# Kernel tuning notes

Measured on AMD Instinct MI355X. Metric: run time of the kernel, lower is better.

The kernel has to match this reference:

```python
import jax, jax.numpy as jnp
import numpy as np

EMBED = 1024
HEADS = 16
HEAD_DIM = EMBED // HEADS
SCALE = HEAD_DIM ** -0.5


def setup_inputs() -> dict:
    key = jax.random.key(0)
    ks = jax.random.split(key, 9)
    init = lambda k, shape: jax.random.normal(k, shape, dtype=jnp.float32) * 0.02
    return {
        "hidden_states": jax.random.normal(ks[0], (32, 257, EMBED), dtype=jnp.float32),
        "Wq": init(ks[1], (EMBED, EMBED)), "bq": init(ks[2], (EMBED,)),
        "Wk": init(ks[3], (EMBED, EMBED)), "bk": init(ks[4], (EMBED,)),
        "Wv": init(ks[5], (EMBED, EMBED)), "bv": init(ks[6], (EMBED,)),
        "Wo": init(ks[7], (EMBED, EMBED)), "bo": init(ks[8], (EMBED,)),
    }


def reference(hidden_states, Wq, bq, Wk, bk, Wv, bv, Wo, bo):
    b, t, d = hidden_states.shape
    # projections (torch Linear: x @ W.T + b); scale applied to Q
    q = (hidden_states @ Wq.T + bq) * SCALE
    k = hidden_states @ Wk.T + bk
    v = hidden_states @ Wv.T + bv
    # [b, h, t, hd]
    q = q.reshape(b, t, HEADS, HEAD_DIM).transpose(0, 2, 1, 3)
    k = k.reshape(b, t, HEADS, HEAD_DIM).transpose(0, 2, 1, 3)
    v = v.reshape(b, t, HEADS, HEAD_DIM).transpose(0, 2, 1, 3)
    # attention scores + softmax (dropout p is a no-op in eval mode)
    scores = jnp.einsum("bhqd,bhkd->bhqk", q, k)
    probs = jax.nn.softmax(scores, axis=-1)
    ctx = jnp.einsum("bhqk,bhkd->bhqd", probs, v)
    ctx = ctx.transpose(0, 2, 1, 3).reshape(b, t, d)
    return ctx @ Wo.T + bo
```

## Files before the change

kernel.cpp:

```cpp
#include <hip/hip_runtime.h>


#define B_   32
#define T_   257
#define TP   272
#define H_   16
#define HD_  64
#define D_   1024
#define NTOK 8224
#define BH_  512
#define FRAG_PER_BH 17408

typedef __bf16 bf16;
typedef __bf16 bf16x4 __attribute__((ext_vector_type(4)));
typedef __bf16 bf16x8 __attribute__((ext_vector_type(8)));
typedef short  s16x4  __attribute__((ext_vector_type(4)));
typedef short  s16x8  __attribute__((ext_vector_type(8)));
typedef float  floatx4 __attribute__((ext_vector_type(4)));

static constexpr size_t SZ_XB   = (size_t)NTOK * D_ * 2;
static constexpr size_t SZ_WQKV = (size_t)3 * D_ * D_ * 2;
static constexpr size_t SZ_W    = (size_t)D_ * D_ * 2;
static constexpr size_t SZ_QK   = (size_t)BH_ * FRAG_PER_BH * 2;

static constexpr size_t OFF_XB   = 0;
static constexpr size_t OFF_WQKV = OFF_XB + SZ_XB;
static constexpr size_t OFF_WO   = OFF_WQKV + SZ_WQKV;
static constexpr size_t OFF_Q    = OFF_WO + SZ_W;
static constexpr size_t OFF_K    = OFF_Q + SZ_QK;
static constexpr size_t OFF_V    = OFF_K + SZ_QK;
static constexpr size_t OFF_CTX  = OFF_V + SZ_QK;

#define GLD16(gp, lp)                                                        \
  __builtin_amdgcn_global_load_lds(                                          \
      (const __attribute__((address_space(1))) void*)(gp),                   \
      (__attribute__((address_space(3))) void*)(lp), 16, 0, 0)

__global__ void cast_bf16_kernel(const float* __restrict__ src,
                                 bf16* __restrict__ dst, int n4) {
  int i = blockIdx.x * blockDim.x + threadIdx.x;
  int stride = gridDim.x * blockDim.x;
  for (int idx = i; idx < n4; idx += stride) {
    float4 v = reinterpret_cast<const float4*>(src)[idx];
    bf16x4 o;
    o[0] = (bf16)v.x; o[1] = (bf16)v.y; o[2] = (bf16)v.z; o[3] = (bf16)v.w;
    reinterpret_cast<bf16x4*>(dst)[idx] = o;
  }
}

__global__ void cast4_kernel(const float* __restrict__ s0, const float* __restrict__ s1,
                             const float* __restrict__ s2, const float* __restrict__ s3,
                             bf16* __restrict__ d0, bf16* __restrict__ d1,
                             bf16* __restrict__ d2, bf16* __restrict__ d3, int n4) {
  const float* s = (blockIdx.y == 0) ? s0 : (blockIdx.y == 1) ? s1
                   : (blockIdx.y == 2) ? s2 : s3;
  bf16* d = (blockIdx.y == 0) ? d0 : (blockIdx.y == 1) ? d1
            : (blockIdx.y == 2) ? d2 : d3;
  int i = blockIdx.x * blockDim.x + threadIdx.x;
  int stride = gridDim.x * blockDim.x;
  for (int idx = i; idx < n4; idx += stride) {
    float4 v = reinterpret_cast<const float4*>(s)[idx];
    bf16x4 o;
    o[0] = (bf16)v.x; o[1] = (bf16)v.y; o[2] = (bf16)v.z; o[3] = (bf16)v.w;
    reinterpret_cast<bf16x4*>(d)[idx] = o;
  }
}


__global__ __launch_bounds__(256) void qkv_gemm(
    const bf16* __restrict__ xb, const bf16* __restrict__ wqkv,
    const float* __restrict__ bq, const float* __restrict__ bk,
    const float* __restrict__ bv,
    bf16* __restrict__ Qf, bf16* __restrict__ Kf, bf16* __restrict__ Vf) {
  __shared__ bf16 smem[9216];
  bf16* Ash = smem;
  bf16* Bsh = smem + 4096;

  const int linear = blockIdx.x;
  const int nbg = ((linear & 7) * 3 + ((linear >> 3) % 3)) * 128;
  const int mbase = (linear / 24) * 128;
  const int tid = threadIdx.x;
  const int lane = tid & 63;
  const int w = tid >> 6;
  const int wr = w >> 1, wc = w & 1;
  const int n15 = lane & 15, quad = lane >> 4;

  const int lrow = lane >> 2;
  const int lseg = (lane & 3) * 8;

  floatx4 acc[4][4] = {};

  for (int k0 = 0; k0 < D_; k0 += 32) {
#pragma unroll
    for (int c = 0; c < 2; c++) {
      int r0 = w * 32 + c * 16;
      int row = r0 + lrow;
      int gm = mbase + row; if (gm > NTOK - 1) gm = NTOK - 1;
      GLD16(xb + (size_t)gm * D_ + k0 + lseg, Ash + r0 * 32);
      GLD16(wqkv + (size_t)(nbg + row) * D_ + k0 + lseg, Bsh + r0 * 32);
    }
    __syncthreads();
    bf16x8 af[4], bfr[4];
#pragma unroll
    for (int i = 0; i < 4; i++) {
      af[i]  = *reinterpret_cast<const bf16x8*>(Ash + (wr * 64 + i * 16 + n15) * 32 + quad * 8);
      bfr[i] = *reinterpret_cast<const bf16x8*>(Bsh + (wc * 64 + i * 16 + n15) * 32 + quad * 8);
    }
#pragma unroll
    for (int i = 0; i < 4; i++)
#pragma unroll
      for (int j = 0; j < 4; j++)
        acc[i][j] = __builtin_amdgcn_mfma_f32_16x16x32_bf16(af[i], bfr[j], acc[i][j], 0, 0, 0);
    __syncthreads();
  }

  const int z = nbg >> 10;
  bf16* zdst = (z == 0) ? Qf : (z == 1) ? Kf : Vf;
  const float scale = (z == 0) ? 0.125f : 1.0f;
  const float* bias = (z == 0) ? bq : (z == 1) ? bk : bv;
  const int zoff = nbg & 1023;

  const int bA = mbase / T_;
  const int tA = mbase - bA * T_;
  const int tEndA = (tA + 128 < T_) ? tA + 128 : T_;
  const int tgA0 = tA >> 4;
  const int nA = ((tEndA - 1) >> 4) - tgA0 + 1;
  int nU = nA, tEndB = 0;
  if (tA + 128 > T_ && bA + 1 < B_) {
    tEndB = tA + 128 - T_;
    nU += ((tEndB - 1) >> 4) + 1;
  }

  for (int half = 0; half < 2; half++) {
    if (wc == half) {
#pragma unroll
      for (int i = 0; i < 4; i++)
#pragma unroll
        for (int j = 0; j < 4; j++) {
          int colL = j * 16 + n15;
          float bval = bias[zoff + half * 64 + colL];
#pragma unroll
          for (int r = 0; r < 4; r++) {
            int rowL = wr * 64 + i * 16 + quad * 4 + r;
            smem[rowL * 72 + colL] = (bf16)((acc[i][j][r] + bval) * scale);
          }
        }
    }
    __syncthreads();
    const int h = (zoff >> 6) + half;
    for (int u = w; u < nU; u += 4) {
      int b, tg, tlo, thi;
      if (u < nA) {
        b = bA; tg = tgA0 + u;
        tlo = (tA > tg * 16) ? tA : tg * 16;
        int te = tg * 16 + 16; thi = (te < tEndA) ? te : tEndA;
      } else {
        b = bA + 1; tg = u - nA;
        tlo = tg * 16;
        int te = tg * 16 + 16; thi = (te < tEndB) ? te : tEndB;
      }
      bf16* gb = zdst + (size_t)(b * H_ + h) * FRAG_PER_BH + tg * 1024;
      if (z != 2) {
        int ki = lane & 15, dc = lane >> 4;
        int t = tg * 16 + ki;
        if (t >= tlo && t < thi) {
          int rowL = b * T_ + t - mbase;
          bf16x8 v0 = *reinterpret_cast<const bf16x8*>(smem + rowL * 72 + dc * 8);
          bf16x8 v1 = *reinterpret_cast<const bf16x8*>(smem + rowL * 72 + 32 + dc * 8);
          *reinterpret_cast<bf16x8*>(gb + dc * 128 + ki * 8) = v0;
          *reinterpret_cast<bf16x8*>(gb + 512 + dc * 128 + ki * 8) = v1;
        }
      } else {
        int q2 = (lane >> 4) & 3, d16 = lane & 15;
        int tb = tg * 16 + q2 * 4;
        bool full = (tb >= tlo) && (tb + 3 < thi);
#pragma unroll
        for (int p = 0; p < 2; p++) {
          bf16x8 vv;
#pragma unroll
          for (int dp = 0; dp < 2; dp++)
#pragma unroll
            for (int ki = 0; ki < 4; ki++) {
              int t = tb + ki;
              int rr = (b * T_ + t - mbase) & 127;
              vv[dp * 4 + ki] = smem[rr * 72 + p * 32 + dp * 16 + d16];
            }
          bf16* cp = gb + (p * 4 + q2) * 128 + d16 * 8;
          if (full) {
            *reinterpret_cast<bf16x8*>(cp) = vv;
          } else {
#pragma unroll
            for (int dp = 0; dp < 2; dp++)
#pragma unroll
              for (int ki = 0; ki < 4; ki++) {
                int t = tb + ki;
                if (t >= tlo && t < thi) cp[dp * 4 + ki] = vv[dp * 4 + ki];
              }
          }
        }
      }
    }
    __syncthreads();
  }
}

__global__ __launch_bounds__(256) void attn_kernel(
    const bf16* __restrict__ Qf, const bf16* __restrict__ Kf,
    const bf16* __restrict__ Vf, bf16* __restrict__ ctx) {
  __shared__ bf16 smem[34816];

  const int bh = blockIdx.x;
  const int tid = threadIdx.x;
  const int lane = tid & 63, w = tid >> 6;
  const int n15 = lane & 15, quad = lane >> 4;
  const int b = bh >> 4, h = bh & 15;

  const bf16* Qb = Qf + (size_t)bh * FRAG_PER_BH;
  const bf16* Kb = Kf + (size_t)bh * FRAG_PER_BH;
  const bf16* Vb = Vf + (size_t)bh * FRAG_PER_BH;

#pragma unroll
  for (int j = 0; j < 17; j++) {
    int c = w * 17 + j;
    const bf16* src = (c < 34) ? (Kb + c * 512) : (Vb + (c - 34) * 512);
    GLD16(src + lane * 8, smem + c * 512);
  }
  __syncthreads();
  const bf16* Ksh = smem;
  const bf16* Vsh = smem + 17408;

  const int fo = quad * 128 + n15 * 8;

  for (int qt = w; qt < 17; qt += 4) {
    bf16x8 qb0 = *reinterpret_cast<const bf16x8*>(Qb + qt * 1024 + fo);
    bf16x8 qb1 = *reinterpret_cast<const bf16x8*>(Qb + qt * 1024 + 512 + fo);

    floatx4 s[17];
#pragma unroll
    for (int kt = 0; kt < 17; kt++) {
      bf16x8 ka0 = *reinterpret_cast<const bf16x8*>(Ksh + kt * 1024 + fo);
      bf16x8 ka1 = *reinterpret_cast<const bf16x8*>(Ksh + kt * 1024 + 512 + fo);
      floatx4 c = {};
      c = __builtin_amdgcn_mfma_f32_16x16x32_bf16(ka0, qb0, c, 0, 0, 0);
      c = __builtin_amdgcn_mfma_f32_16x16x32_bf16(ka1, qb1, c, 0, 0, 0);
      s[kt] = c;
    }
    s[16][1] = -1e30f; s[16][2] = -1e30f; s[16][3] = -1e30f;
    if (quad != 0) s[16][0] = -1e30f;

    float m0 = -1e30f;
#pragma unroll
    for (int kt = 0; kt < 17; kt++)
#pragma unroll
      for (int r = 0; r < 4; r++) m0 = fmaxf(m0, s[kt][r]);
    m0 = fmaxf(m0, __shfl_xor(m0, 16));
    m0 = fmaxf(m0, __shfl_xor(m0, 32));

    float sum = 0.f;
    s16x4 pb[17];
#pragma unroll
    for (int kt = 0; kt < 17; kt++) {
      bf16x4 ph;
#pragma unroll
      for (int r = 0; r < 4; r++) {
        float p = __expf(s[kt][r] - m0);
        sum += p;
        ph[r] = (bf16)p;
      }
      pb[kt] = __builtin_bit_cast(s16x4, ph);
    }
    sum += __shfl_xor(sum, 16);
    sum += __shfl_xor(sum, 32);

    floatx4 o[4] = {};
#pragma unroll
    for (int kt = 0; kt < 17; kt++) {
#pragma unroll
      for (int p = 0; p < 2; p++) {
        bf16x8 vv = *reinterpret_cast<const bf16x8*>(
            Vsh + ((kt * 2 + p) * 4 + quad) * 128 + n15 * 8);
        s16x8 v16 = __builtin_bit_cast(s16x8, vv);
        s16x4 vlo = __builtin_shufflevector(v16, v16, 0, 1, 2, 3);
        s16x4 vhi = __builtin_shufflevector(v16, v16, 4, 5, 6, 7);
        o[p * 2]     = __builtin_amdgcn_mfma_f32_16x16x16bf16_1k(vlo, pb[kt], o[p * 2], 0, 0, 0);
        o[p * 2 + 1] = __builtin_amdgcn_mfma_f32_16x16x16bf16_1k(vhi, pb[kt], o[p * 2 + 1], 0, 0, 0);
      }
    }

    int q = qt * 16 + n15;
    if (q < T_) {
      float inv = 1.0f / sum;
      size_t ob = ((size_t)(b * T_ + q)) * D_ + h * 64 + quad * 4;
#pragma unroll
      for (int dt = 0; dt < 4; dt++) {
        bf16x4 ov;
#pragma unroll
        for (int r = 0; r < 4; r++) ov[r] = (bf16)(o[dt][r] * inv);
        *reinterpret_cast<bf16x4*>(ctx + ob + dt * 16) = ov;
      }
    }
  }
}

__global__ __launch_bounds__(256) void o_gemm(
    const bf16* __restrict__ ctx, const bf16* __restrict__ wo,
    const float* __restrict__ bo, float* __restrict__ out) {
  __shared__ bf16 Ash[128 * 32];
  __shared__ bf16 Bsh[128 * 32];

  const int linear = blockIdx.x;
  const int nbase = (linear & 7) * 128;
  const int mbase = (linear >> 3) * 128;
  const int tid = threadIdx.x;
  const int lane = tid & 63;
  const int w = tid >> 6;
  const int wr = w >> 1, wc = w & 1;
  const int n15 = lane & 15, quad = lane >> 4;

  const int lrow = lane >> 2;
  const int lseg = (lane & 3) * 8;

  floatx4 acc[4][4] = {};

  for (int k0 = 0; k0 < D_; k0 += 32) {
#pragma unroll
    for (int c = 0; c < 2; c++) {
      int r0 = w * 32 + c * 16;
      int row = r0 + lrow;
      int gm = mbase + row; if (gm > NTOK - 1) gm = NTOK - 1;
      GLD16(ctx + (size_t)gm * D_ + k0 + lseg, Ash + r0 * 32);
      GLD16(wo + (size_t)(nbase + row) * D_ + k0 + lseg, Bsh + r0 * 32);
    }
    __syncthreads();
    bf16x8 af[4], bfr[4];
#pragma unroll
    for (int i = 0; i < 4; i++) {
      af[i]  = *reinterpret_cast<const bf16x8*>(Ash + (wr * 64 + i * 16 + n15) * 32 + quad * 8);
      bfr[i] = *reinterpret_cast<const bf16x8*>(Bsh + (wc * 64 + i * 16 + n15) * 32 + quad * 8);
    }
#pragma unroll
    for (int i = 0; i < 4; i++)
#pragma unroll
      for (int j = 0; j < 4; j++)
        acc[i][j] = __builtin_amdgcn_mfma_f32_16x16x32_bf16(af[i], bfr[j], acc[i][j], 0, 0, 0);
    __syncthreads();
  }

#pragma unroll
  for (int i = 0; i < 4; i++) {
    int rowb = mbase + wr * 64 + i * 16 + quad * 4;
#pragma unroll
    for (int j = 0; j < 4; j++) {
      int col = nbase + wc * 64 + j * 16 + n15;
      float bval = bo[col];
#pragma unroll
      for (int r = 0; r < 4; r++) {
        int m = rowb + r;
        if (m < NTOK) out[(size_t)m * D_ + col] = acc[i][j][r] + bval;
      }
    }
  }
}

extern "C" void kernel_launch(void* const* d_in, const int* in_sizes, int n_in,
                              void* d_out, int out_size, void* d_ws, size_t ws_size,
                              hipStream_t stream) {
  const float* hs = (const float*)d_in[0];
  const float* Wq = (const float*)d_in[1];
  const float* bq = (const float*)d_in[2];
  const float* Wk = (const float*)d_in[3];
  const float* bk = (const float*)d_in[4];
  const float* Wv = (const float*)d_in[5];
  const float* bv = (const float*)d_in[6];
  const float* Wo = (const float*)d_in[7];
  const float* bo = (const float*)d_in[8];

  char* ws = (char*)d_ws;
  bf16* xb   = (bf16*)(ws + OFF_XB);
  bf16* wqkv = (bf16*)(ws + OFF_WQKV);
  bf16* wob  = (bf16*)(ws + OFF_WO);
  bf16* Qfw  = (bf16*)(ws + OFF_Q);
  bf16* Kfw  = (bf16*)(ws + OFF_K);
  bf16* Vfw  = (bf16*)(ws + OFF_V);
  bf16* ctx  = (bf16*)(ws + OFF_CTX);

  cast_bf16_kernel<<<2048, 256, 0, stream>>>(hs, xb, NTOK * D_ / 4);
  cast4_kernel<<<dim3(256, 4), 256, 0, stream>>>(
      Wq, Wk, Wv, Wo,
      wqkv, wqkv + (size_t)D_ * D_, wqkv + (size_t)2 * D_ * D_, wob,
      D_ * D_ / 4);

  qkv_gemm<<<1560, 256, 0, stream>>>(xb, wqkv, bq, bk, bv, Qfw, Kfw, Vfw);
  attn_kernel<<<BH_, 256, 0, stream>>>(Qfw, Kfw, Vfw, ctx);
  o_gemm<<<520, 256, 0, stream>>>(ctx, wob, bo, (float*)d_out);
}
```

Baseline: 252.1 us.

## Widen GEMM K-tiles with XOR-swizzled LDS, split attention query tiles, use exp2

Both GEMMs now load 64-wide K tiles per iteration into an XOR-swizzled LDS layout, which halves the barrier count and is meant to avoid bank conflicts on fragment reads. The attention kernel splits each (batch, head) across two blocks over query tiles, keeps only K in LDS, and reads V directly from global memory. It also prefetches the next Q fragment. The softmax scale now folds in log2(e) so exp2f replaces __expf. The attention changes double occupancy opportunity but load K twice and rely on cache for the uncached V reads.

```diff
diff --git a/kernel.cpp b/kernel.cpp
--- a/kernel.cpp
+++ b/kernel.cpp
@@ -30,6 +30,8 @@
 static constexpr size_t OFF_K    = OFF_Q + SZ_QK;
 static constexpr size_t OFF_V    = OFF_K + SZ_QK;
 static constexpr size_t OFF_CTX  = OFF_V + SZ_QK;
+
+#define QSCALE 0.18033688011112042f
 
 #define GLD16(gp, lp)                                                        \
   __builtin_amdgcn_global_load_lds(                                          \
@@ -72,9 +74,9 @@
     const float* __restrict__ bq, const float* __restrict__ bk,
     const float* __restrict__ bv,
     bf16* __restrict__ Qf, bf16* __restrict__ Kf, bf16* __restrict__ Vf) {
-  __shared__ bf16 smem[9216];
+  __shared__ bf16 smem[16384];
   bf16* Ash = smem;
-  bf16* Bsh = smem + 4096;
+  bf16* Bsh = smem + 8192;
 
   const int linear = blockIdx.x;
   const int nbg = ((linear & 7) * 3 + ((linear >> 3) % 3)) * 128;
@@ -85,38 +87,47 @@
   const int wr = w >> 1, wc = w & 1;
   const int n15 = lane & 15, quad = lane >> 4;
 
-  const int lrow = lane >> 2;
-  const int lseg = (lane & 3) * 8;
+  const int r8 = lane >> 3;
+  const int sG = ((lane & 7) ^ r8) * 8;
 
   floatx4 acc[4][4] = {};
 
-  for (int k0 = 0; k0 < D_; k0 += 32) {
-#pragma unroll
-    for (int c = 0; c < 2; c++) {
-      int r0 = w * 32 + c * 16;
-      int row = r0 + lrow;
-      int gm = mbase + row; if (gm > NTOK - 1) gm = NTOK - 1;
-      GLD16(xb + (size_t)gm * D_ + k0 + lseg, Ash + r0 * 32);
-      GLD16(wqkv + (size_t)(nbg + row) * D_ + k0 + lseg, Bsh + r0 * 32);
-    }
-    __syncthreads();
-    bf16x8 af[4], bfr[4];
+  for (int k0 = 0; k0 < D_; k0 += 64) {
+#pragma unroll
+    for (int c = 0; c < 4; c++) {
+      int rbase = c * 32 + w * 8;
+      int rloc = rbase + r8;
+      int gm = mbase + rloc; if (gm > NTOK - 1) gm = NTOK - 1;
+      GLD16(xb + (size_t)gm * D_ + k0 + sG, Ash + rbase * 64);
+      GLD16(wqkv + (size_t)(nbg + rloc) * D_ + k0 + sG, Bsh + rbase * 64);
+    }
+    __syncthreads();
+    bf16x8 af[4][2], bfr[4][2];
+    const int sw = n15 & 7;
 #pragma unroll
     for (int i = 0; i < 4; i++) {
-      af[i]  = *reinterpret_cast<const bf16x8*>(Ash + (wr * 64 + i * 16 + n15) * 32 + quad * 8);
-      bfr[i] = *reinterpret_cast<const bf16x8*>(Bsh + (wc * 64 + i * 16 + n15) * 32 + quad * 8);
+      int arow = (wr * 64 + i * 16 + n15) * 64;
+      int brow = (wc * 64 + i * 16 + n15) * 64;
+#pragma unroll
+      for (int hh = 0; hh < 2; hh++) {
+        int so = ((hh * 4 + quad) ^ sw) * 8;
+        af[i][hh]  = *reinterpret_cast<const bf16x8*>(Ash + arow + so);
+        bfr[i][hh] = *reinterpret_cast<const bf16x8*>(Bsh + brow + so);
+      }
     }
 #pragma unroll
     for (int i = 0; i < 4; i++)
 #pragma unroll
-      for (int j = 0; j < 4; j++)
-        acc[i][j] = __builtin_amdgcn_mfma_f32_16x16x32_bf16(af[i], bfr[j], acc[i][j], 0, 0, 0);
+      for (int j = 0; j < 4; j++) {
+        acc[i][j] = __builtin_amdgcn_mfma_f32_16x16x32_bf16(af[i][0], bfr[j][0], acc[i][j], 0, 0, 0);
+        acc[i][j] = __builtin_amdgcn_mfma_f32_16x16x32_bf16(af[i][1], bfr[j][1], acc[i][j], 0, 0, 0);
+      }
     __syncthreads();
   }
 
   const int z = nbg >> 10;
   bf16* zdst = (z == 0) ? Qf : (z == 1) ? Kf : Vf;
-  const float scale = (z == 0) ? 0.125f : 1.0f;
+  const float scale = (z == 0) ? QSCALE : 1.0f;
   const float* bias = (z == 0) ? bq : (z == 1) ? bk : bv;
   const int zoff = nbg & 1023;
 
@@ -207,9 +218,10 @@
 __global__ __launch_bounds__(256) void attn_kernel(
     const bf16* __restrict__ Qf, const bf16* __restrict__ Kf,
     const bf16* __restrict__ Vf, bf16* __restrict__ ctx) {
-  __shared__ bf16 smem[34816];
-
-  const int bh = blockIdx.x;
+  __shared__ bf16 Ksh[17408];
+
+  const int bid = blockIdx.x;
+  const int bh = bid >> 1, z = bid & 1;
   const int tid = threadIdx.x;
   const int lane = tid & 63, w = tid >> 6;
   const int n15 = lane & 15, quad = lane >> 4;
@@ -219,21 +231,26 @@
   const bf16* Kb = Kf + (size_t)bh * FRAG_PER_BH;
   const bf16* Vb = Vf + (size_t)bh * FRAG_PER_BH;
 
-#pragma unroll
-  for (int j = 0; j < 17; j++) {
-    int c = w * 17 + j;
-    const bf16* src = (c < 34) ? (Kb + c * 512) : (Vb + (c - 34) * 512);
-    GLD16(src + lane * 8, smem + c * 512);
-  }
+  for (int j = w; j < 34; j += 4) GLD16(Kb + j * 512 + lane * 8, Ksh + j * 512);
   __syncthreads();
-  const bf16* Ksh = smem;
-  const bf16* Vsh = smem + 17408;
 
   const int fo = quad * 128 + n15 * 8;
-
-  for (int qt = w; qt < 17; qt += 4) {
-    bf16x8 qb0 = *reinterpret_cast<const bf16x8*>(Qb + qt * 1024 + fo);
-    bf16x8 qb1 = *reinterpret_cast<const bf16x8*>(Qb + qt * 1024 + 512 + fo);
+  const int lo = z ? 9 : 0, hi = z ? 17 : 9;
+
+  const int qt0 = lo + w;
+  bf16x8 cq0 = {}, cq1 = {};
+  if (qt0 < hi) {
+    cq0 = *reinterpret_cast<const bf16x8*>(Qb + qt0 * 1024 + fo);
+    cq1 = *reinterpret_cast<const bf16x8*>(Qb + qt0 * 1024 + 512 + fo);
+  }
+
+  for (int qt = qt0; qt < hi; qt += 4) {
+    const int nqt = qt + 4;
+    bf16x8 nq0 = {}, nq1 = {};
+    if (nqt < hi) {
+      nq0 = *reinterpret_cast<const bf16x8*>(Qb + nqt * 1024 + fo);
+      nq1 = *reinterpret_cast<const bf16x8*>(Qb + nqt * 1024 + 512 + fo);
+    }
 
     floatx4 s[17];
 #pragma unroll
@@ -241,8 +258,8 @@
       bf16x8 ka0 = *reinterpret_cast<const bf16x8*>(Ksh + kt * 1024 + fo);
       bf16x8 ka1 = *reinterpret_cast<const bf16x8*>(Ksh + kt * 1024 + 512 + fo);
       floatx4 c = {};
-      c = __builtin_amdgcn_mfma_f32_16x16x32_bf16(ka0, qb0, c, 0, 0, 0);
-      c = __builtin_amdgcn_mfma_f32_16x16x32_bf16(ka1, qb1, c, 0, 0, 0);
+      c = __builtin_amdgcn_mfma_f32_16x16x32_bf16(ka0, cq0, c, 0, 0, 0);
+      c = __builtin_amdgcn_mfma_f32_16x16x32_bf16(ka1, cq1, c, 0, 0, 0);
       s[kt] = c;
     }
     s[16][1] = -1e30f; s[16][2] = -1e30f; s[16][3] = -1e30f;
@@ -263,7 +280,7 @@
       bf16x4 ph;
 #pragma unroll
       for (int r = 0; r < 4; r++) {
-        float p = __expf(s[kt][r] - m0);
+        float p = exp2f(s[kt][r] - m0);
         sum += p;
         ph[r] = (bf16)p;
       }
@@ -278,7 +295,7 @@
 #pragma unroll
       for (int p = 0; p < 2; p++) {
         bf16x8 vv = *reinterpret_cast<const bf16x8*>(
-            Vsh + ((kt * 2 + p) * 4 + quad) * 128 + n15 * 8);
+            Vb + ((kt * 2 + p) * 4 + quad) * 128 + n15 * 8);
         s16x8 v16 = __builtin_bit_cast(s16x8, vv);
         s16x4 vlo = __builtin_shufflevector(v16, v16, 0, 1, 2, 3);
         s16x4 vhi = __builtin_shufflevector(v16, v16, 4, 5, 6, 7);
@@ -299,14 +316,16 @@
         *reinterpret_cast<bf16x4*>(ctx + ob + dt * 16) = ov;
       }
     }
+    cq0 = nq0; cq1 = nq1;
   }
 }
 
 __global__ __launch_bounds__(256) void o_gemm(
     const bf16* __restrict__ ctx, const bf16* __restrict__ wo,
     const float* __restrict__ bo, float* __restrict__ out) {
-  __shared__ bf16 Ash[128 * 32];
-  __shared__ bf16 Bsh[128 * 32];
+  __shared__ bf16 smem[16384];
+  bf16* Ash = smem;
+  bf16* Bsh = smem + 8192;
 
   const int linear = blockIdx.x;
   const int nbase = (linear & 7) * 128;
@@ -317,32 +336,41 @@
   const int wr = w >> 1, wc = w & 1;
   const int n15 = lane & 15, quad = lane >> 4;
 
-  const int lrow = lane >> 2;
-  const int lseg = (lane & 3) * 8;
+  const int r8 = lane >> 3;
+  const int sG = ((lane & 7) ^ r8) * 8;
 
   floatx4 acc[4][4] = {};
 
-  for (int k0 = 0; k0 < D_; k0 += 32) {
-#pragma unroll
-    for (int c = 0; c < 2; c++) {
-      int r0 = w * 32 + c * 16;
-      int row = r0 + lrow;
-      int gm = mbase + row; if (gm > NTOK - 1) gm = NTOK - 1;
-      GLD16(ctx + (size_t)gm * D_ + k0 + lseg, Ash + r0 * 32);
-      GLD16(wo + (size_t)(nbase + row) * D_ + k0 + lseg, Bsh + r0 * 32);
-    }
-    __syncthreads();
-    bf16x8 af[4], bfr[4];
+  for (int k0 = 0; k0 < D_; k0 += 64) {
+#pragma unroll
+    for (int c = 0; c < 4; c++) {
+      int rbase = c * 32 + w * 8;
+      int rloc = rbase + r8;
+      int gm = mbase + rloc; if (gm > NTOK - 1) gm = NTOK - 1;
+      GLD16(ctx + (size_t)gm * D_ + k0 + sG, Ash + rbase * 64);
+      GLD16(wo + (size_t)(nbase + rloc) * D_ + k0 + sG, Bsh + rbase * 64);
+    }
+    __syncthreads();
+    bf16x8 af[4][2], bfr[4][2];
+    const int sw = n15 & 7;
 #pragma unroll
     for (int i = 0; i < 4; i++) {
-      af[i]  = *reinterpret_cast<const bf16x8*>(Ash + (wr * 64 + i * 16 + n15) * 32 + quad * 8);
-      bfr[i] = *reinterpret_cast<const bf16x8*>(Bsh + (wc * 64 + i * 16 + n15) * 32 + quad * 8);
+      int arow = (wr * 64 + i * 16 + n15) * 64;
+      int brow = (wc * 64 + i * 16 + n15) * 64;
+#pragma unroll
+      for (int hh = 0; hh < 2; hh++) {
+        int so = ((hh * 4 + quad) ^ sw) * 8;
+        af[i][hh]  = *reinterpret_cast<const bf16x8*>(Ash + arow + so);
+        bfr[i][hh] = *reinterpret_cast<const bf16x8*>(Bsh + brow + so);
+      }
     }
 #pragma unroll
     for (int i = 0; i < 4; i++)
 #pragma unroll
-      for (int j = 0; j < 4; j++)
-        acc[i][j] = __builtin_amdgcn_mfma_f32_16x16x32_bf16(af[i], bfr[j], acc[i][j], 0, 0, 0);
+      for (int j = 0; j < 4; j++) {
+        acc[i][j] = __builtin_amdgcn_mfma_f32_16x16x32_bf16(af[i][0], bfr[j][0], acc[i][j], 0, 0, 0);
+        acc[i][j] = __builtin_amdgcn_mfma_f32_16x16x32_bf16(af[i][1], bfr[j][1], acc[i][j], 0, 0, 0);
+      }
     __syncthreads();
   }
 
@@ -391,6 +419,6 @@
       D_ * D_ / 4);
 
   qkv_gemm<<<1560, 256, 0, stream>>>(xb, wqkv, bq, bk, bv, Qfw, Kfw, Vfw);
-  attn_kernel<<<BH_, 256, 0, stream>>>(Qfw, Kfw, Vfw, ctx);
+  attn_kernel<<<1024, 256, 0, stream>>>(Qfw, Kfw, Vfw, ctx);
   o_gemm<<<520, 256, 0, stream>>>(ctx, wob, bo, (float*)d_out);
 }
```

Result: slower. 282.9 us (+12.2%).

## Widen attention to 8 waves, fold log2e into Q scale, halve o_gemm M tile

Applied to the files above, without the earlier changes.

Attention blocks grow from 4 to 8 waves, so each wave handles at most 3 query tiles instead of 5, and the next Q fragment is prefetched into registers. The Q scale now includes log2(e), which lets softmax use exp2f in place of __expf. The output GEMM tile shrinks from 128 to 64 rows, roughly doubling the grid to 1032 blocks for better CU fill. The trade-offs are more blocks, less reuse per block in o_gemm, and register pressure under the new 512-thread launch bounds.

```diff
diff --git a/kernel.cpp b/kernel.cpp
--- a/kernel.cpp
+++ b/kernel.cpp
@@ -30,6 +30,8 @@
 static constexpr size_t OFF_K    = OFF_Q + SZ_QK;
 static constexpr size_t OFF_V    = OFF_K + SZ_QK;
 static constexpr size_t OFF_CTX  = OFF_V + SZ_QK;
+
+#define QSCALE 0.18033688011112042f
 
 #define GLD16(gp, lp)                                                        \
   __builtin_amdgcn_global_load_lds(                                          \
@@ -116,7 +118,7 @@
 
   const int z = nbg >> 10;
   bf16* zdst = (z == 0) ? Qf : (z == 1) ? Kf : Vf;
-  const float scale = (z == 0) ? 0.125f : 1.0f;
+  const float scale = (z == 0) ? QSCALE : 1.0f;
   const float* bias = (z == 0) ? bq : (z == 1) ? bk : bv;
   const int zoff = nbg & 1023;
 
@@ -204,7 +206,7 @@
   }
 }
 
-__global__ __launch_bounds__(256) void attn_kernel(
+__global__ __launch_bounds__(512, 4) void attn_kernel(
     const bf16* __restrict__ Qf, const bf16* __restrict__ Kf,
     const bf16* __restrict__ Vf, bf16* __restrict__ ctx) {
   __shared__ bf16 smem[34816];
@@ -219,9 +221,7 @@
   const bf16* Kb = Kf + (size_t)bh * FRAG_PER_BH;
   const bf16* Vb = Vf + (size_t)bh * FRAG_PER_BH;
 
-#pragma unroll
-  for (int j = 0; j < 17; j++) {
-    int c = w * 17 + j;
+  for (int c = w; c < 68; c += 8) {
     const bf16* src = (c < 34) ? (Kb + c * 512) : (Vb + (c - 34) * 512);
     GLD16(src + lane * 8, smem + c * 512);
   }
@@ -231,9 +231,16 @@
 
   const int fo = quad * 128 + n15 * 8;
 
-  for (int qt = w; qt < 17; qt += 4) {
-    bf16x8 qb0 = *reinterpret_cast<const bf16x8*>(Qb + qt * 1024 + fo);
-    bf16x8 qb1 = *reinterpret_cast<const bf16x8*>(Qb + qt * 1024 + 512 + fo);
+  bf16x8 cq0 = *reinterpret_cast<const bf16x8*>(Qb + w * 1024 + fo);
+  bf16x8 cq1 = *reinterpret_cast<const bf16x8*>(Qb + w * 1024 + 512 + fo);
+
+  for (int qt = w; qt < 17; qt += 8) {
+    const int nqt = qt + 8;
+    bf16x8 nq0 = {}, nq1 = {};
+    if (nqt < 17) {
+      nq0 = *reinterpret_cast<const bf16x8*>(Qb + nqt * 1024 + fo);
+      nq1 = *reinterpret_cast<const bf16x8*>(Qb + nqt * 1024 + 512 + fo);
+    }
 
     floatx4 s[17];
 #pragma unroll
@@ -241,8 +248,8 @@
       bf16x8 ka0 = *reinterpret_cast<const bf16x8*>(Ksh + kt * 1024 + fo);
       bf16x8 ka1 = *reinterpret_cast<const bf16x8*>(Ksh + kt * 1024 + 512 + fo);
       floatx4 c = {};
-      c = __builtin_amdgcn_mfma_f32_16x16x32_bf16(ka0, qb0, c, 0, 0, 0);
-      c = __builtin_amdgcn_mfma_f32_16x16x32_bf16(ka1, qb1, c, 0, 0, 0);
+      c = __builtin_amdgcn_mfma_f32_16x16x32_bf16(ka0, cq0, c, 0, 0, 0);
+      c = __builtin_amdgcn_mfma_f32_16x16x32_bf16(ka1, cq1, c, 0, 0, 0);
       s[kt] = c;
     }
     s[16][1] = -1e30f; s[16][2] = -1e30f; s[16][3] = -1e30f;
@@ -263,7 +270,7 @@
       bf16x4 ph;
 #pragma unroll
       for (int r = 0; r < 4; r++) {
-        float p = __expf(s[kt][r] - m0);
+        float p = exp2f(s[kt][r] - m0);
         sum += p;
         ph[r] = (bf16)p;
       }
@@ -299,18 +306,19 @@
         *reinterpret_cast<bf16x4*>(ctx + ob + dt * 16) = ov;
       }
     }
+    cq0 = nq0; cq1 = nq1;
   }
 }
 
 __global__ __launch_bounds__(256) void o_gemm(
     const bf16* __restrict__ ctx, const bf16* __restrict__ wo,
     const float* __restrict__ bo, float* __restrict__ out) {
-  __shared__ bf16 Ash[128 * 32];
+  __shared__ bf16 Ash[64 * 32];
   __shared__ bf16 Bsh[128 * 32];
 
   const int linear = blockIdx.x;
   const int nbase = (linear & 7) * 128;
-  const int mbase = (linear >> 3) * 128;
+  const int mbase = (linear >> 3) * 64;
   const int tid = threadIdx.x;
   const int lane = tid & 63;
   const int w = tid >> 6;
@@ -320,26 +328,29 @@
   const int lrow = lane >> 2;
   const int lseg = (lane & 3) * 8;
 
-  floatx4 acc[4][4] = {};
+  floatx4 acc[2][4] = {};
 
   for (int k0 = 0; k0 < D_; k0 += 32) {
+    {
+      int r0 = w * 16;
+      int gm = mbase + r0 + lrow; if (gm > NTOK - 1) gm = NTOK - 1;
+      GLD16(ctx + (size_t)gm * D_ + k0 + lseg, Ash + r0 * 32);
+    }
 #pragma unroll
     for (int c = 0; c < 2; c++) {
       int r0 = w * 32 + c * 16;
-      int row = r0 + lrow;
-      int gm = mbase + row; if (gm > NTOK - 1) gm = NTOK - 1;
-      GLD16(ctx + (size_t)gm * D_ + k0 + lseg, Ash + r0 * 32);
-      GLD16(wo + (size_t)(nbase + row) * D_ + k0 + lseg, Bsh + r0 * 32);
-    }
-    __syncthreads();
-    bf16x8 af[4], bfr[4];
-#pragma unroll
-    for (int i = 0; i < 4; i++) {
-      af[i]  = *reinterpret_cast<const bf16x8*>(Ash + (wr * 64 + i * 16 + n15) * 32 + quad * 8);
-      bfr[i] = *reinterpret_cast<const bf16x8*>(Bsh + (wc * 64 + i * 16 + n15) * 32 + quad * 8);
-    }
-#pragma unroll
-    for (int i = 0; i < 4; i++)
+      GLD16(wo + (size_t)(nbase + r0 + lrow) * D_ + k0 + lseg, Bsh + r0 * 32);
+    }
+    __syncthreads();
+    bf16x8 af[2], bfr[4];
+#pragma unroll
+    for (int i = 0; i < 2; i++)
+      af[i] = *reinterpret_cast<const bf16x8*>(Ash + (wr * 32 + i * 16 + n15) * 32 + quad * 8);
+#pragma unroll
+    for (int j = 0; j < 4; j++)
+      bfr[j] = *reinterpret_cast<const bf16x8*>(Bsh + (wc * 64 + j * 16 + n15) * 32 + quad * 8);
+#pragma unroll
+    for (int i = 0; i < 2; i++)
 #pragma unroll
       for (int j = 0; j < 4; j++)
         acc[i][j] = __builtin_amdgcn_mfma_f32_16x16x32_bf16(af[i], bfr[j], acc[i][j], 0, 0, 0);
@@ -347,8 +358,8 @@
   }
 
 #pragma unroll
-  for (int i = 0; i < 4; i++) {
-    int rowb = mbase + wr * 64 + i * 16 + quad * 4;
+  for (int i = 0; i < 2; i++) {
+    int rowb = mbase + wr * 32 + i * 16 + quad * 4;
 #pragma unroll
     for (int j = 0; j < 4; j++) {
       int col = nbase + wc * 64 + j * 16 + n15;
@@ -391,6 +402,6 @@
       D_ * D_ / 4);
 
   qkv_gemm<<<1560, 256, 0, stream>>>(xb, wqkv, bq, bk, bv, Qfw, Kfw, Vfw);
-  attn_kernel<<<BH_, 256, 0, stream>>>(Qfw, Kfw, Vfw, ctx);
-  o_gemm<<<520, 256, 0, stream>>>(ctx, wob, bo, (float*)d_out);
-}
+  attn_kernel<<<BH_, 512, 0, stream>>>(Qfw, Kfw, Vfw, ctx);
+  o_gemm<<<1032, 256, 0, stream>>>(ctx, wob, bo, (float*)d_out);
+}
```

Result: slower. 421.8 us (+67.3%).
